# Performance work log

Measured on AMD Instinct MI355X. Metric: run time of the kernel, lower is better.

The kernel has to match this reference:

```python
import jax, jax.numpy as jnp
import numpy as np
import math

D_MODEL = 1024
NUM_HEADS = 16
ROPE_THETA = 10000.0
BATCH = 4
SEQ = 2048


def apply_rope(x, pos, theta=ROPE_THETA):
    # x: (b, h, s, d_k), pos: (s,) int positions
    d = x.shape[-1]
    inv_freq = theta ** (-jnp.arange(0, d, 2, dtype=jnp.float32) / d)  # (d/2,)
    ang = pos.astype(jnp.float32)[:, None] * inv_freq                  # (s, d/2)
    cos, sin = jnp.cos(ang), jnp.sin(ang)
    x1, x2 = x[..., 0::2], x[..., 1::2]
    # interleave rotated pairs back to last dim
    out = jnp.stack([x1 * cos - x2 * sin, x1 * sin + x2 * cos], axis=-1)
    return out.reshape(x.shape)


def setup_inputs() -> dict:
    key = jax.random.key(0)
    ks = jax.random.split(key, 5)
    scale = 1.0 / math.sqrt(D_MODEL)
    return {
        "x": jax.random.normal(ks[0], (BATCH, SEQ, D_MODEL), dtype=jnp.float32),
        "token_positions": jnp.arange(SEQ, dtype=jnp.int64 if jax.config.jax_enable_x64 else jnp.int32),
        "Wq": jax.random.normal(ks[1], (D_MODEL, D_MODEL), dtype=jnp.float32) * scale,
        "Wk": jax.random.normal(ks[2], (D_MODEL, D_MODEL), dtype=jnp.float32) * scale,
        "Wv": jax.random.normal(ks[3], (D_MODEL, D_MODEL), dtype=jnp.float32) * scale,
        "Wo": jax.random.normal(ks[4], (D_MODEL, D_MODEL), dtype=jnp.float32) * scale,
    }


def reference(x, token_positions, Wq, Wk, Wv, Wo):
    b, s, d_model = x.shape
    h = NUM_HEADS
    d_k = d_model // h

    def proj_split(W):
        # Linear: y = x @ W.T (W is (out,in)); then split heads -> (b, h, s, d_k)
        y = jnp.einsum('bsi,oi->bso', x, W)
        return y.reshape(b, s, h, d_k).transpose(0, 2, 1, 3)

    q = apply_rope(proj_split(Wq), token_positions)
    k = apply_rope(proj_split(Wk), token_positions)
    v = proj_split(Wv)

    scores = jnp.einsum('bhqd,bhkd->bhqk', q, k) / jnp.asarray(math.sqrt(d_k), x.dtype)
    causal = jnp.tril(jnp.ones((s, s), dtype=bool))  # (s, s) keep lower triangle
    scores = jnp.where(causal, scores, jnp.asarray(-jnp.inf, scores.dtype))
    attn = jax.nn.softmax(scores, axis=-1)
    out = jnp.einsum('bhqk,bhkd->bhqd', attn, v)
    out = out.transpose(0, 2, 1, 3).reshape(b, s, d_model)
    return jnp.einsum('bsi,oi->bso', out, Wo)
```

## Files before the change

### kernel.cpp

```cpp
#include <hip/hip_runtime.h>
#include <cstdint>
#include <cstddef>


typedef __attribute__((ext_vector_type(8))) short bf16x8;
typedef __attribute__((ext_vector_type(4))) float f32x4;

#define LOG2E 1.4426950408889634f

__device__ __forceinline__ unsigned short f2bf(float f) {
  unsigned int u = __builtin_bit_cast(unsigned int, f);
  unsigned int r = (u + 0x7FFFu + ((u >> 16) & 1u)) >> 16;
  return (unsigned short)r;
}
__device__ __forceinline__ float bf2f(unsigned short h) {
  return __builtin_bit_cast(float, (unsigned int)h << 16);
}
__device__ __forceinline__ unsigned int packbf2(float a, float b) {
  return (unsigned int)f2bf(a) | ((unsigned int)f2bf(b) << 16);
}
__device__ __forceinline__ int swz(int idx) {
  return idx ^ (((idx >> 6) & 7) << 3);
}

__global__ __launch_bounds__(256) void cvt_kernel(const float* __restrict__ in,
                                                  unsigned short* __restrict__ out,
                                                  int n8) {
  int i = blockIdx.x * 256 + threadIdx.x;
  if (i < n8) {
    float4 u0 = ((const float4*)in)[i * 2];
    float4 u1 = ((const float4*)in)[i * 2 + 1];
    uint4 v = {packbf2(u0.x, u0.y), packbf2(u0.z, u0.w),
               packbf2(u1.x, u1.y), packbf2(u1.z, u1.w)};
    ((uint4*)out)[i] = v;
  }
}
__global__ __launch_bounds__(256) void cvt_w3(const float* __restrict__ w0,
                                              const float* __restrict__ w1,
                                              const float* __restrict__ w2,
                                              unsigned short* __restrict__ dst) {
  const float* src = blockIdx.y == 0 ? w0 : (blockIdx.y == 1 ? w1 : w2);
  unsigned short* d = dst + (size_t)blockIdx.y * 1024 * 1024;
  int i = blockIdx.x * 256 + threadIdx.x;
  float4 u0 = ((const float4*)src)[i * 2];
  float4 u1 = ((const float4*)src)[i * 2 + 1];
  uint4 v = {packbf2(u0.x, u0.y), packbf2(u0.z, u0.w),
             packbf2(u1.x, u1.y), packbf2(u1.z, u1.w)};
  ((uint4*)d)[i] = v;
}

__global__ __launch_bounds__(256) void gemm_qkv(const unsigned short* __restrict__ Xb,
                                                const unsigned short* __restrict__ Wb3,
                                                unsigned short* __restrict__ Qb,
                                                unsigned short* __restrict__ Kb,
                                                unsigned short* __restrict__ Vtb) {
  __shared__ alignas(16) unsigned short As[128 * 64];
  __shared__ alignas(16) unsigned short Bs[128 * 64];
  const int t = threadIdx.x;
  const int lane = t & 63;
  const int w = t >> 6;
  const int wr = w >> 1, wc = w & 1;
  const int fr = lane & 15, fq = lane >> 4;
  const int m0 = blockIdx.x * 128;
  const int sel = blockIdx.y >> 3;
  const int n0 = (blockIdx.y & 7) * 128;
  const unsigned short* Wp = Wb3 + (size_t)sel * 1024 * 1024;
  const int K = 1024;

  const f32x4 zero = {0.f, 0.f, 0.f, 0.f};
  f32x4 acc[4][4];
#pragma unroll
  for (int m = 0; m < 4; ++m)
#pragma unroll
    for (int n = 0; n < 4; ++n) acc[m][n] = zero;

  for (int k0 = 0; k0 < K; k0 += 64) {
#pragma unroll
    for (int cc = 0; cc < 4; ++cc) {
      int c = w * 4 + cc;
      int flat = c * 512 + lane * 8;
      int row = flat >> 6, col = flat & 63;
      __builtin_amdgcn_global_load_lds(
          (const __attribute__((address_space(1))) void*)(Xb + (size_t)(m0 + row) * K + (k0 + col)),
          (__attribute__((address_space(3))) void*)&As[c * 512], 16, 0, 0);
      __builtin_amdgcn_global_load_lds(
          (const __attribute__((address_space(1))) void*)(Wp + (size_t)(n0 + row) * K + (k0 + col)),
          (__attribute__((address_space(3))) void*)&Bs[c * 512], 16, 0, 0);
    }
    __syncthreads();
#pragma unroll
    for (int kk = 0; kk < 2; ++kk) {
      bf16x8 a[4], b[4];
#pragma unroll
      for (int m = 0; m < 4; ++m)
        a[m] = *(const bf16x8*)&As[(wr * 64 + m * 16 + fr) * 64 + kk * 32 + fq * 8];
#pragma unroll
      for (int n = 0; n < 4; ++n)
        b[n] = *(const bf16x8*)&Bs[(wc * 64 + n * 16 + fr) * 64 + kk * 32 + fq * 8];
#pragma unroll
      for (int m = 0; m < 4; ++m)
#pragma unroll
        for (int n = 0; n < 4; ++n)
          acc[m][n] = __builtin_amdgcn_mfma_f32_16x16x32_bf16(a[m], b[n], acc[m][n], 0, 0, 0);
    }
    __syncthreads();
  }

#pragma unroll
  for (int m = 0; m < 4; ++m)
#pragma unroll
    for (int n = 0; n < 4; ++n) {
      int row = m0 + wr * 64 + m * 16 + fq * 4;
      int col = n0 + wc * 64 + n * 16 + fr;
      if (sel < 2) {
        unsigned short* Cp = sel ? Kb : Qb;
#pragma unroll
        for (int j = 0; j < 4; ++j)
          Cp[(size_t)(row + j) * 1024 + col] = f2bf(acc[m][n][j]);
      } else {
        int b = row >> 11, s = row & 2047;
        int h = col >> 6, d = col & 63;
        ushort4 v4 = {f2bf(acc[m][n][0]), f2bf(acc[m][n][1]),
                      f2bf(acc[m][n][2]), f2bf(acc[m][n][3])};
        *(ushort4*)&Vtb[(((size_t)b * 16 + h) * 64 + d) * 2048 + s] = v4;
      }
    }
}

__global__ __launch_bounds__(256) void rope_kernel(unsigned short* __restrict__ Q,
                                                   unsigned short* __restrict__ Kb,
                                                   const int* __restrict__ tp) {
  int idx = blockIdx.x * 256 + threadIdx.x;
  unsigned short* ptr = blockIdx.y ? Kb : Q;
  const float scale = blockIdx.y ? 1.0f : 0.125f * LOG2E;
  int flat8 = idx * 8;
  int r = flat8 >> 10;
  int colbase = flat8 & 1023;
  int ibase = (colbase & 63) >> 1;
  int s = r & 2047;
  float pos = (float)tp[s];
  const float cexp = -13.287712379549449f / 32.0f;

  uint4 v = *(const uint4*)&ptr[flat8];
  unsigned int* vp = (unsigned int*)&v;
  uint4 o;
  unsigned int* op = (unsigned int*)&o;
#pragma unroll
  for (int p = 0; p < 4; ++p) {
    float inv = exp2f((float)(ibase + p) * cexp);
    float ang = pos * inv;
    float sn, cs;
    sincosf(ang, &sn, &cs);
    float x1 = bf2f((unsigned short)(vp[p] & 0xFFFFu));
    float x2 = bf2f((unsigned short)(vp[p] >> 16));
    op[p] = packbf2((x1 * cs - x2 * sn) * scale, (x1 * sn + x2 * cs) * scale);
  }
  *(uint4*)&ptr[flat8] = o;
}

__global__ __launch_bounds__(256) void attn_kernel(const unsigned short* __restrict__ Q,
                                                   const unsigned short* __restrict__ K,
                                                   const unsigned short* __restrict__ Vt_g,
                                                   unsigned short* __restrict__ O) {
  __shared__ alignas(16) unsigned short Ks[64 * 64];
  __shared__ alignas(16) unsigned short Vt[64 * 64];
  const int t = threadIdx.x;
  const int lane = t & 63, w = t >> 6;
  const int fr = lane & 15, fq = lane >> 4;
  const int h = blockIdx.y, b = blockIdx.z;
  const size_t base = ((size_t)b * 2048) * 1024 + (size_t)h * 64;
  const size_t vbase = ((size_t)b * 16 + h) * 64 * 2048;
  const f32x4 zero = {0.f, 0.f, 0.f, 0.f};

  for (int pass = 0; pass < 2; ++pass) {
    const int qt = pass ? (31 - blockIdx.x) : blockIdx.x;
    const int q0 = qt * 64;

    bf16x8 qf[2];
#pragma unroll
    for (int kk = 0; kk < 2; ++kk)
      qf[kk] = *(const bf16x8*)&Q[base + (size_t)(q0 + w * 16 + fr) * 1024 + kk * 32 + fq * 8];

    float m_ = -INFINITY, l_ = 0.f;
    f32x4 oaccT[4];
#pragma unroll
    for (int n = 0; n < 4; ++n) oaccT[n] = zero;

    uint4 kr[2], vr[2];
#pragma unroll
    for (int it = 0; it < 2; ++it) {
      int flat = it * 2048 + t * 8;
      int row = flat >> 6, col = flat & 63;
      kr[it] = *(const uint4*)&K[base + (size_t)row * 1024 + col];
      vr[it] = *(const uint4*)&Vt_g[vbase + (size_t)row * 2048 + col];
    }

    for (int kv0 = 0; kv0 <= q0; kv0 += 64) {
      __syncthreads();
#pragma unroll
      for (int it = 0; it < 2; ++it) {
        int flat = it * 2048 + t * 8;
        *(uint4*)&Ks[swz(flat)] = kr[it];
        *(uint4*)&Vt[swz(flat)] = vr[it];
      }
      __syncthreads();
      if (kv0 + 64 <= q0) {
#pragma unroll
        for (int it = 0; it < 2; ++it) {
          int flat = it * 2048 + t * 8;
          int row = flat >> 6, col = flat & 63;
          kr[it] = *(const uint4*)&K[base + (size_t)(kv0 + 64 + row) * 1024 + col];
          vr[it] = *(const uint4*)&Vt_g[vbase + (size_t)row * 2048 + kv0 + 64 + col];
        }
      }

      f32x4 sa[4];
#pragma unroll
      for (int n = 0; n < 4; ++n) sa[n] = zero;
#pragma unroll
      for (int kk = 0; kk < 2; ++kk) {
#pragma unroll
        for (int n = 0; n < 4; ++n) {
          bf16x8 kf = *(const bf16x8*)&Ks[swz((n * 16 + fr) * 64 + kk * 32 + fq * 8)];
          sa[n] = __builtin_amdgcn_mfma_f32_16x16x32_bf16(kf, qf[kk], sa[n], 0, 0, 0);
        }
      }

      const bool diag = (kv0 == q0);
      float pmax = -3.0e38f;
#pragma unroll
      for (int n = 0; n < 4; ++n)
#pragma unroll
        for (int j = 0; j < 4; ++j) {
          float s = sa[n][j];
          if (diag && (n * 16 + fq * 4 + j > w * 16 + fr)) s = -3.0e38f;
          sa[n][j] = s;
          pmax = fmaxf(pmax, s);
        }
      pmax = fmaxf(pmax, __shfl_xor(pmax, 16));
      pmax = fmaxf(pmax, __shfl_xor(pmax, 32));
      float mn = fmaxf(m_, pmax);
      float alpha = exp2f(m_ - mn);
      m_ = mn;
      float ps = 0.f;
#pragma unroll
      for (int n = 0; n < 4; ++n)
#pragma unroll
        for (int j = 0; j < 4; ++j) {
          float e = exp2f(sa[n][j] - mn);
          sa[n][j] = e;
          ps += e;
        }
      ps += __shfl_xor(ps, 16);
      ps += __shfl_xor(ps, 32);
      l_ = l_ * alpha + ps;
#pragma unroll
      for (int n = 0; n < 4; ++n)
#pragma unroll
        for (int j = 0; j < 4; ++j) oaccT[n][j] *= alpha;

      unsigned R[4][2], F[4][2];
#pragma unroll
      for (int n = 0; n < 4; ++n)
#pragma unroll
        for (int pp = 0; pp < 2; ++pp)
          R[n][pp] = packbf2(sa[n][2 * pp], sa[n][2 * pp + 1]);
#pragma unroll
      for (int pp = 0; pp < 2; ++pp) {
        unsigned t0 = (fq < 2) ? R[1][pp] : R[0][pp];
        unsigned t1 = (fq < 2) ? R[3][pp] : R[2][pp];
        t0 = (unsigned)__shfl_xor((int)t0, 32);
        t1 = (unsigned)__shfl_xor((int)t1, 32);
        unsigned G0 = (fq < 2) ? R[0][pp] : t0;
        unsigned G1 = (fq < 2) ? t0 : R[1][pp];
        unsigned G2 = (fq < 2) ? R[2][pp] : t1;
        unsigned G3 = (fq < 2) ? t1 : R[3][pp];
        unsigned u0 = ((fq & 1) == 0) ? G1 : G0;
        unsigned u1 = ((fq & 1) == 0) ? G3 : G2;
        u0 = (unsigned)__shfl_xor((int)u0, 16);
        u1 = (unsigned)__shfl_xor((int)u1, 16);
        F[0][pp] = ((fq & 1) == 0) ? G0 : u0;
        F[1][pp] = ((fq & 1) == 0) ? u0 : G1;
        F[2][pp] = ((fq & 1) == 0) ? G2 : u1;
        F[3][pp] = ((fq & 1) == 0) ? u1 : G3;
      }
      union U8 { unsigned u[4]; bf16x8 v; };
      U8 pb0, pb1;
      pb0.u[0] = F[0][0]; pb0.u[1] = F[0][1]; pb0.u[2] = F[1][0]; pb0.u[3] = F[1][1];
      pb1.u[0] = F[2][0]; pb1.u[1] = F[2][1]; pb1.u[2] = F[3][0]; pb1.u[3] = F[3][1];

#pragma unroll
      for (int n = 0; n < 4; ++n) {
        bf16x8 vf0 = *(const bf16x8*)&Vt[swz((n * 16 + fr) * 64 + 0 * 32 + fq * 8)];
        oaccT[n] = __builtin_amdgcn_mfma_f32_16x16x32_bf16(vf0, pb0.v, oaccT[n], 0, 0, 0);
        bf16x8 vf1 = *(const bf16x8*)&Vt[swz((n * 16 + fr) * 64 + 1 * 32 + fq * 8)];
        oaccT[n] = __builtin_amdgcn_mfma_f32_16x16x32_bf16(vf1, pb1.v, oaccT[n], 0, 0, 0);
      }
    }

    float rl = 1.0f / l_;
#pragma unroll
    for (int n = 0; n < 4; ++n) {
      ushort4 v4 = {f2bf(oaccT[n][0] * rl), f2bf(oaccT[n][1] * rl),
                    f2bf(oaccT[n][2] * rl), f2bf(oaccT[n][3] * rl)};
      *(ushort4*)&O[base + (size_t)(q0 + w * 16 + fr) * 1024 + n * 16 + fq * 4] = v4;
    }
  }
}

__global__ __launch_bounds__(256) void gemm_out(const unsigned short* __restrict__ Ap,
                                                const float* __restrict__ Wp,
                                                float* __restrict__ Cp) {
  __shared__ alignas(16) unsigned short As[128 * 64];
  __shared__ alignas(16) unsigned short Bs[128 * 64];
  const int t = threadIdx.x;
  const int lane = t & 63;
  const int w = t >> 6;
  const int wr = w >> 1, wc = w & 1;
  const int fr = lane & 15, fq = lane >> 4;
  const int m0 = blockIdx.x * 128, n0 = blockIdx.y * 128;
  const int K = 1024, N = 1024;

  const f32x4 zero = {0.f, 0.f, 0.f, 0.f};
  f32x4 acc[4][4];
#pragma unroll
  for (int m = 0; m < 4; ++m)
#pragma unroll
    for (int n = 0; n < 4; ++n) acc[m][n] = zero;

  for (int k0 = 0; k0 < K; k0 += 64) {
#pragma unroll
    for (int cc = 0; cc < 4; ++cc) {
      int c = w * 4 + cc;
      int flat = c * 512 + lane * 8;
      int row = flat >> 6, col = flat & 63;
      __builtin_amdgcn_global_load_lds(
          (const __attribute__((address_space(1))) void*)(Ap + (size_t)(m0 + row) * K + (k0 + col)),
          (__attribute__((address_space(3))) void*)&As[c * 512], 16, 0, 0);
    }
#pragma unroll
    for (int it = 0; it < 4; ++it) {
      int flat = it * 2048 + t * 8;
      int row = flat >> 6, col = flat & 63;
      const float* g = Wp + (size_t)(n0 + row) * K + (k0 + col);
      float4 u0 = *(const float4*)g;
      float4 u1 = *(const float4*)(g + 4);
      uint4 v = {packbf2(u0.x, u0.y), packbf2(u0.z, u0.w),
                 packbf2(u1.x, u1.y), packbf2(u1.z, u1.w)};
      *(uint4*)&Bs[swz(flat)] = v;
    }
    __syncthreads();
#pragma unroll
    for (int kk = 0; kk < 2; ++kk) {
      bf16x8 a[4], b[4];
#pragma unroll
      for (int m = 0; m < 4; ++m)
        a[m] = *(const bf16x8*)&As[(wr * 64 + m * 16 + fr) * 64 + kk * 32 + fq * 8];
#pragma unroll
      for (int n = 0; n < 4; ++n)
        b[n] = *(const bf16x8*)&Bs[swz((wc * 64 + n * 16 + fr) * 64 + kk * 32 + fq * 8)];
#pragma unroll
      for (int m = 0; m < 4; ++m)
#pragma unroll
        for (int n = 0; n < 4; ++n)
          acc[m][n] = __builtin_amdgcn_mfma_f32_16x16x32_bf16(a[m], b[n], acc[m][n], 0, 0, 0);
    }
    __syncthreads();
  }

#pragma unroll
  for (int m = 0; m < 4; ++m)
#pragma unroll
    for (int n = 0; n < 4; ++n) {
      int row = m0 + wr * 64 + m * 16 + fq * 4;
      int col = n0 + wc * 64 + n * 16 + fr;
#pragma unroll
      for (int j = 0; j < 4; ++j)
        Cp[(size_t)(row + j) * N + col] = acc[m][n][j];
    }
}

extern "C" void kernel_launch(void* const* d_in, const int* in_sizes, int n_in,
                              void* d_out, int out_size, void* d_ws, size_t ws_size,
                              hipStream_t stream) {
  const float* x  = (const float*)d_in[0];
  const int* tp   = (const int*)d_in[1];
  const float* Wq = (const float*)d_in[2];
  const float* Wk = (const float*)d_in[3];
  const float* Wv = (const float*)d_in[4];
  const float* Wo = (const float*)d_in[5];
  float* out = (float*)d_out;

  const size_t MAT = (size_t)8192 * 1024;
  unsigned short* Qb  = (unsigned short*)d_ws;
  unsigned short* Kb  = Qb + MAT;
  unsigned short* Vtb = Kb + MAT;
  unsigned short* Xb  = Vtb + MAT;
  unsigned short* Ob  = Xb;
  unsigned short* Wb3 = (unsigned short*)d_out;

  cvt_kernel<<<4096, 256, 0, stream>>>(x, Xb, 8192 * 1024 / 8);
  cvt_w3<<<dim3(512, 3), 256, 0, stream>>>(Wq, Wk, Wv, Wb3);
  gemm_qkv<<<dim3(64, 24), 256, 0, stream>>>(Xb, Wb3, Qb, Kb, Vtb);
  rope_kernel<<<dim3(4096, 2), 256, 0, stream>>>(Qb, Kb, tp);
  attn_kernel<<<dim3(16, 16, 4), 256, 0, stream>>>(Qb, Kb, Vtb, Ob);
  gemm_out<<<dim3(64, 8), 256, 0, stream>>>(Ob, Wo, out);
}
```

Measured before the change: 409.7 us.

## Restructure attention to 256-row query tiles with 8 waves; pre-convert Wo to bf16

The attention kernel now uses 512-thread blocks covering 256 query rows, with each wave handling two 16-row groups. Each staged K/V tile is reused across more queries, and fully masked groups are skipped. The grid is remapped so the heavy and light causal tiles are interleaved, replacing the earlier two-pass pairing scheme. The output GEMM now reads a bf16 copy of Wo, produced by a separate conversion into the freed Q buffer, and loads it straight into LDS with global_load_lds without swizzle. This trades possible LDS bank conflicts and load imbalance across waves for fewer global reloads and less fp32 traffic.

Result: no change. 413.4 us (+0.9%).

```diff
diff --git a/kernel.cpp b/kernel.cpp
--- a/kernel.cpp
+++ b/kernel.cpp
@@ -158,159 +158,167 @@
   *(uint4*)&ptr[flat8] = o;
 }
 
-__global__ __launch_bounds__(256) void attn_kernel(const unsigned short* __restrict__ Q,
-                                                   const unsigned short* __restrict__ K,
-                                                   const unsigned short* __restrict__ Vt_g,
-                                                   unsigned short* __restrict__ O) {
+__global__ __launch_bounds__(512, 2) void attn_kernel(const unsigned short* __restrict__ Q,
+                                                      const unsigned short* __restrict__ K,
+                                                      const unsigned short* __restrict__ Vt_g,
+                                                      unsigned short* __restrict__ O) {
   __shared__ alignas(16) unsigned short Ks[64 * 64];
   __shared__ alignas(16) unsigned short Vt[64 * 64];
   const int t = threadIdx.x;
   const int lane = t & 63, w = t >> 6;
   const int fr = lane & 15, fq = lane >> 4;
-  const int h = blockIdx.y, b = blockIdx.z;
+  const int gblk = (blockIdx.x & 7) * 64 + (blockIdx.x >> 3);
+  const int qt = gblk & 7;
+  const int hb = gblk >> 3;
+  const int h = hb & 15, b = hb >> 4;
+  const int q0 = qt * 256;
   const size_t base = ((size_t)b * 2048) * 1024 + (size_t)h * 64;
   const size_t vbase = ((size_t)b * 16 + h) * 64 * 2048;
   const f32x4 zero = {0.f, 0.f, 0.f, 0.f};
 
-  for (int pass = 0; pass < 2; ++pass) {
-    const int qt = pass ? (31 - blockIdx.x) : blockIdx.x;
-    const int q0 = qt * 64;
-
-    bf16x8 qf[2];
+  bf16x8 qf[2][2];
+#pragma unroll
+  for (int g = 0; g < 2; ++g)
 #pragma unroll
     for (int kk = 0; kk < 2; ++kk)
-      qf[kk] = *(const bf16x8*)&Q[base + (size_t)(q0 + w * 16 + fr) * 1024 + kk * 32 + fq * 8];
-
-    float m_ = -INFINITY, l_ = 0.f;
-    f32x4 oaccT[4];
-#pragma unroll
-    for (int n = 0; n < 4; ++n) oaccT[n] = zero;
-
-    uint4 kr[2], vr[2];
-#pragma unroll
-    for (int it = 0; it < 2; ++it) {
-      int flat = it * 2048 + t * 8;
-      int row = flat >> 6, col = flat & 63;
-      kr[it] = *(const uint4*)&K[base + (size_t)row * 1024 + col];
-      vr[it] = *(const uint4*)&Vt_g[vbase + (size_t)row * 2048 + col];
-    }
-
-    for (int kv0 = 0; kv0 <= q0; kv0 += 64) {
-      __syncthreads();
-#pragma unroll
-      for (int it = 0; it < 2; ++it) {
-        int flat = it * 2048 + t * 8;
-        *(uint4*)&Ks[swz(flat)] = kr[it];
-        *(uint4*)&Vt[swz(flat)] = vr[it];
-      }
-      __syncthreads();
-      if (kv0 + 64 <= q0) {
-#pragma unroll
-        for (int it = 0; it < 2; ++it) {
-          int flat = it * 2048 + t * 8;
-          int row = flat >> 6, col = flat & 63;
-          kr[it] = *(const uint4*)&K[base + (size_t)(kv0 + 64 + row) * 1024 + col];
-          vr[it] = *(const uint4*)&Vt_g[vbase + (size_t)row * 2048 + kv0 + 64 + col];
+      qf[g][kk] = *(const bf16x8*)&Q[base + (size_t)(q0 + w * 32 + g * 16 + fr) * 1024 + kk * 32 + fq * 8];
+
+  float m_[2] = {-INFINITY, -INFINITY};
+  float l_[2] = {0.f, 0.f};
+  f32x4 oaccT[2][4];
+#pragma unroll
+  for (int g = 0; g < 2; ++g)
+#pragma unroll
+    for (int n = 0; n < 4; ++n) oaccT[g][n] = zero;
+
+  const int sflat = t * 8;
+  const int srow = sflat >> 6, scol = sflat & 63;
+  const int sdst = swz(sflat);
+  uint4 kr = *(const uint4*)&K[base + (size_t)srow * 1024 + scol];
+  uint4 vr = *(const uint4*)&Vt_g[vbase + (size_t)srow * 2048 + scol];
+  const int kvend = q0 + 256;
+  const int wq = q0 + w * 32;
+
+  for (int kv0 = 0; kv0 < kvend; kv0 += 64) {
+    __syncthreads();
+    *(uint4*)&Ks[sdst] = kr;
+    *(uint4*)&Vt[sdst] = vr;
+    __syncthreads();
+    if (kv0 + 64 < kvend) {
+      kr = *(const uint4*)&K[base + (size_t)(kv0 + 64 + srow) * 1024 + scol];
+      vr = *(const uint4*)&Vt_g[vbase + (size_t)srow * 2048 + kv0 + 64 + scol];
+    }
+
+    if (kv0 <= wq + 31) {
+      bf16x8 kf[2][4];
+#pragma unroll
+      for (int kk = 0; kk < 2; ++kk)
+#pragma unroll
+        for (int n = 0; n < 4; ++n)
+          kf[kk][n] = *(const bf16x8*)&Ks[swz((n * 16 + fr) * 64 + kk * 32 + fq * 8)];
+
+#pragma unroll
+      for (int g = 0; g < 2; ++g) {
+        if (kv0 > wq + g * 16 + 15) continue;
+        f32x4 sa[4];
+#pragma unroll
+        for (int n = 0; n < 4; ++n) sa[n] = zero;
+#pragma unroll
+        for (int kk = 0; kk < 2; ++kk)
+#pragma unroll
+          for (int n = 0; n < 4; ++n)
+            sa[n] = __builtin_amdgcn_mfma_f32_16x16x32_bf16(kf[kk][n], qf[g][kk], sa[n], 0, 0, 0);
+
+        const int dd = kv0 - wq - g * 16;
+        const bool diag = (dd > -63);
+        float pmax = -3.0e38f;
+#pragma unroll
+        for (int n = 0; n < 4; ++n)
+#pragma unroll
+          for (int j = 0; j < 4; ++j) {
+            float s = sa[n][j];
+            if (diag && (n * 16 + fq * 4 + j + dd > fr)) s = -3.0e38f;
+            sa[n][j] = s;
+            pmax = fmaxf(pmax, s);
+          }
+        pmax = fmaxf(pmax, __shfl_xor(pmax, 16));
+        pmax = fmaxf(pmax, __shfl_xor(pmax, 32));
+        float mn = fmaxf(m_[g], pmax);
+        float alpha = exp2f(m_[g] - mn);
+        m_[g] = mn;
+        float ps = 0.f;
+#pragma unroll
+        for (int n = 0; n < 4; ++n)
+#pragma unroll
+          for (int j = 0; j < 4; ++j) {
+            float e = exp2f(sa[n][j] - mn);
+            sa[n][j] = e;
+            ps += e;
+          }
+        ps += __shfl_xor(ps, 16);
+        ps += __shfl_xor(ps, 32);
+        l_[g] = l_[g] * alpha + ps;
+#pragma unroll
+        for (int n = 0; n < 4; ++n)
+#pragma unroll
+          for (int j = 0; j < 4; ++j) oaccT[g][n][j] *= alpha;
+
+        unsigned R[4][2], F[4][2];
+#pragma unroll
+        for (int n = 0; n < 4; ++n)
+#pragma unroll
+          for (int pp = 0; pp < 2; ++pp)
+            R[n][pp] = packbf2(sa[n][2 * pp], sa[n][2 * pp + 1]);
+#pragma unroll
+        for (int pp = 0; pp < 2; ++pp) {
+          unsigned t0 = (fq < 2) ? R[1][pp] : R[0][pp];
+          unsigned t1 = (fq < 2) ? R[3][pp] : R[2][pp];
+          t0 = (unsigned)__shfl_xor((int)t0, 32);
+          t1 = (unsigned)__shfl_xor((int)t1, 32);
+          unsigned G0 = (fq < 2) ? R[0][pp] : t0;
+          unsigned G1 = (fq < 2) ? t0 : R[1][pp];
+          unsigned G2 = (fq < 2) ? R[2][pp] : t1;
+          unsigned G3 = (fq < 2) ? t1 : R[3][pp];
+          unsigned u0 = ((fq & 1) == 0) ? G1 : G0;
+          unsigned u1 = ((fq & 1) == 0) ? G3 : G2;
+          u0 = (unsigned)__shfl_xor((int)u0, 16);
+          u1 = (unsigned)__shfl_xor((int)u1, 16);
+          F[0][pp] = ((fq & 1) == 0) ? G0 : u0;
+          F[1][pp] = ((fq & 1) == 0) ? u0 : G1;
+          F[2][pp] = ((fq & 1) == 0) ? G2 : u1;
+          F[3][pp] = ((fq & 1) == 0) ? u1 : G3;
+        }
+        union U8 { unsigned u[4]; bf16x8 v; };
+        U8 pb0, pb1;
+        pb0.u[0] = F[0][0]; pb0.u[1] = F[0][1]; pb0.u[2] = F[1][0]; pb0.u[3] = F[1][1];
+        pb1.u[0] = F[2][0]; pb1.u[1] = F[2][1]; pb1.u[2] = F[3][0]; pb1.u[3] = F[3][1];
+
+#pragma unroll
+        for (int n = 0; n < 4; ++n) {
+          bf16x8 vf0 = *(const bf16x8*)&Vt[swz((n * 16 + fr) * 64 + 0 * 32 + fq * 8)];
+          oaccT[g][n] = __builtin_amdgcn_mfma_f32_16x16x32_bf16(vf0, pb0.v, oaccT[g][n], 0, 0, 0);
+          bf16x8 vf1 = *(const bf16x8*)&Vt[swz((n * 16 + fr) * 64 + 1 * 32 + fq * 8)];
+          oaccT[g][n] = __builtin_amdgcn_mfma_f32_16x16x32_bf16(vf1, pb1.v, oaccT[g][n], 0, 0, 0);
         }
       }
-
-      f32x4 sa[4];
-#pragma unroll
-      for (int n = 0; n < 4; ++n) sa[n] = zero;
-#pragma unroll
-      for (int kk = 0; kk < 2; ++kk) {
-#pragma unroll
-        for (int n = 0; n < 4; ++n) {
-          bf16x8 kf = *(const bf16x8*)&Ks[swz((n * 16 + fr) * 64 + kk * 32 + fq * 8)];
-          sa[n] = __builtin_amdgcn_mfma_f32_16x16x32_bf16(kf, qf[kk], sa[n], 0, 0, 0);
-        }
-      }
-
-      const bool diag = (kv0 == q0);
-      float pmax = -3.0e38f;
-#pragma unroll
-      for (int n = 0; n < 4; ++n)
-#pragma unroll
-        for (int j = 0; j < 4; ++j) {
-          float s = sa[n][j];
-          if (diag && (n * 16 + fq * 4 + j > w * 16 + fr)) s = -3.0e38f;
-          sa[n][j] = s;
-          pmax = fmaxf(pmax, s);
-        }
-      pmax = fmaxf(pmax, __shfl_xor(pmax, 16));
-      pmax = fmaxf(pmax, __shfl_xor(pmax, 32));
-      float mn = fmaxf(m_, pmax);
-      float alpha = exp2f(m_ - mn);
-      m_ = mn;
-      float ps = 0.f;
-#pragma unroll
-      for (int n = 0; n < 4; ++n)
-#pragma unroll
-        for (int j = 0; j < 4; ++j) {
-          float e = exp2f(sa[n][j] - mn);
-          sa[n][j] = e;
-          ps += e;
-        }
-      ps += __shfl_xor(ps, 16);
-      ps += __shfl_xor(ps, 32);
-      l_ = l_ * alpha + ps;
-#pragma unroll
-      for (int n = 0; n < 4; ++n)
-#pragma unroll
-        for (int j = 0; j < 4; ++j) oaccT[n][j] *= alpha;
-
-      unsigned R[4][2], F[4][2];
-#pragma unroll
-      for (int n = 0; n < 4; ++n)
-#pragma unroll
-        for (int pp = 0; pp < 2; ++pp)
-          R[n][pp] = packbf2(sa[n][2 * pp], sa[n][2 * pp + 1]);
-#pragma unroll
-      for (int pp = 0; pp < 2; ++pp) {
-        unsigned t0 = (fq < 2) ? R[1][pp] : R[0][pp];
-        unsigned t1 = (fq < 2) ? R[3][pp] : R[2][pp];
-        t0 = (unsigned)__shfl_xor((int)t0, 32);
-        t1 = (unsigned)__shfl_xor((int)t1, 32);
-        unsigned G0 = (fq < 2) ? R[0][pp] : t0;
-        unsigned G1 = (fq < 2) ? t0 : R[1][pp];
-        unsigned G2 = (fq < 2) ? R[2][pp] : t1;
-        unsigned G3 = (fq < 2) ? t1 : R[3][pp];
-        unsigned u0 = ((fq & 1) == 0) ? G1 : G0;
-        unsigned u1 = ((fq & 1) == 0) ? G3 : G2;
-        u0 = (unsigned)__shfl_xor((int)u0, 16);
-        u1 = (unsigned)__shfl_xor((int)u1, 16);
-        F[0][pp] = ((fq & 1) == 0) ? G0 : u0;
-        F[1][pp] = ((fq & 1) == 0) ? u0 : G1;
-        F[2][pp] = ((fq & 1) == 0) ? G2 : u1;
-        F[3][pp] = ((fq & 1) == 0) ? u1 : G3;
-      }
-      union U8 { unsigned u[4]; bf16x8 v; };
-      U8 pb0, pb1;
-      pb0.u[0] = F[0][0]; pb0.u[1] = F[0][1]; pb0.u[2] = F[1][0]; pb0.u[3] = F[1][1];
-      pb1.u[0] = F[2][0]; pb1.u[1] = F[2][1]; pb1.u[2] = F[3][0]; pb1.u[3] = F[3][1];
-
-#pragma unroll
-      for (int n = 0; n < 4; ++n) {
-        bf16x8 vf0 = *(const bf16x8*)&Vt[swz((n * 16 + fr) * 64 + 0 * 32 + fq * 8)];
-        oaccT[n] = __builtin_amdgcn_mfma_f32_16x16x32_bf16(vf0, pb0.v, oaccT[n], 0, 0, 0);
-        bf16x8 vf1 = *(const bf16x8*)&Vt[swz((n * 16 + fr) * 64 + 1 * 32 + fq * 8)];
-        oaccT[n] = __builtin_amdgcn_mfma_f32_16x16x32_bf16(vf1, pb1.v, oaccT[n], 0, 0, 0);
-      }
-    }
-
-    float rl = 1.0f / l_;
+    }
+  }
+
+#pragma unroll
+  for (int g = 0; g < 2; ++g) {
+    float rl = 1.0f / l_[g];
 #pragma unroll
     for (int n = 0; n < 4; ++n) {
-      ushort4 v4 = {f2bf(oaccT[n][0] * rl), f2bf(oaccT[n][1] * rl),
-                    f2bf(oaccT[n][2] * rl), f2bf(oaccT[n][3] * rl)};
-      *(ushort4*)&O[base + (size_t)(q0 + w * 16 + fr) * 1024 + n * 16 + fq * 4] = v4;
-    }
-  }
-}
-
-__global__ __launch_bounds__(256) void gemm_out(const unsigned short* __restrict__ Ap,
-                                                const float* __restrict__ Wp,
-                                                float* __restrict__ Cp) {
+      ushort4 v4 = {f2bf(oaccT[g][n][0] * rl), f2bf(oaccT[g][n][1] * rl),
+                    f2bf(oaccT[g][n][2] * rl), f2bf(oaccT[g][n][3] * rl)};
+      *(ushort4*)&O[base + (size_t)(q0 + w * 32 + g * 16 + fr) * 1024 + n * 16 + fq * 4] = v4;
+    }
+  }
+}
+
+__global__ __launch_bounds__(256) void gemm_out_bf(const unsigned short* __restrict__ Ap,
+                                                   const unsigned short* __restrict__ Wp,
+                                                   float* __restrict__ Cp) {
   __shared__ alignas(16) unsigned short As[128 * 64];
   __shared__ alignas(16) unsigned short Bs[128 * 64];
   const int t = threadIdx.x;
@@ -337,17 +345,9 @@
       __builtin_amdgcn_global_load_lds(
           (const __attribute__((address_space(1))) void*)(Ap + (size_t)(m0 + row) * K + (k0 + col)),
           (__attribute__((address_space(3))) void*)&As[c * 512], 16, 0, 0);
-    }
-#pragma unroll
-    for (int it = 0; it < 4; ++it) {
-      int flat = it * 2048 + t * 8;
-      int row = flat >> 6, col = flat & 63;
-      const float* g = Wp + (size_t)(n0 + row) * K + (k0 + col);
-      float4 u0 = *(const float4*)g;
-      float4 u1 = *(const float4*)(g + 4);
-      uint4 v = {packbf2(u0.x, u0.y), packbf2(u0.z, u0.w),
-                 packbf2(u1.x, u1.y), packbf2(u1.z, u1.w)};
-      *(uint4*)&Bs[swz(flat)] = v;
+      __builtin_amdgcn_global_load_lds(
+          (const __attribute__((address_space(1))) void*)(Wp + (size_t)(n0 + row) * K + (k0 + col)),
+          (__attribute__((address_space(3))) void*)&Bs[c * 512], 16, 0, 0);
     }
     __syncthreads();
 #pragma unroll
@@ -358,7 +358,7 @@
         a[m] = *(const bf16x8*)&As[(wr * 64 + m * 16 + fr) * 64 + kk * 32 + fq * 8];
 #pragma unroll
       for (int n = 0; n < 4; ++n)
-        b[n] = *(const bf16x8*)&Bs[swz((wc * 64 + n * 16 + fr) * 64 + kk * 32 + fq * 8)];
+        b[n] = *(const bf16x8*)&Bs[(wc * 64 + n * 16 + fr) * 64 + kk * 32 + fq * 8];
 #pragma unroll
       for (int m = 0; m < 4; ++m)
 #pragma unroll
@@ -398,11 +398,13 @@
   unsigned short* Xb  = Vtb + MAT;
   unsigned short* Ob  = Xb;
   unsigned short* Wb3 = (unsigned short*)d_out;
+  unsigned short* WoB = Qb;
 
   cvt_kernel<<<4096, 256, 0, stream>>>(x, Xb, 8192 * 1024 / 8);
   cvt_w3<<<dim3(512, 3), 256, 0, stream>>>(Wq, Wk, Wv, Wb3);
   gemm_qkv<<<dim3(64, 24), 256, 0, stream>>>(Xb, Wb3, Qb, Kb, Vtb);
   rope_kernel<<<dim3(4096, 2), 256, 0, stream>>>(Qb, Kb, tp);
-  attn_kernel<<<dim3(16, 16, 4), 256, 0, stream>>>(Qb, Kb, Vtb, Ob);
-  gemm_out<<<dim3(64, 8), 256, 0, stream>>>(Ob, Wo, out);
-}
+  attn_kernel<<<512, 512, 0, stream>>>(Qb, Kb, Vtb, Ob);
+  cvt_kernel<<<512, 256, 0, stream>>>(Wo, WoB, 1024 * 1024 / 8);
+  gemm_out_bf<<<dim3(64, 8), 256, 0, stream>>>(Ob, WoB, out);
+}
```
